# Performance work log

Hardware: AMD Instinct MI355X
Metric: run time of the kernel (lower is better)

## Reference

```python
import jax, jax.numpy as jnp
import numpy as np

B, L, E, H = 2, 2048, 1024, 16
D = E // H

def setup_inputs() -> dict:
    key = jax.random.key(0)
    ks = jax.random.split(key, 6)
    s = 1.0 / np.sqrt(E)
    return {
        "x": jax.random.normal(ks[0], (B, L, E), dtype=jnp.float32),
        "attention_mask": jnp.ones((B, L), dtype=jnp.float32),
        "Wq": jax.random.normal(ks[1], (E, E), dtype=jnp.float32) * s,
        "Wk": jax.random.normal(ks[2], (E, E), dtype=jnp.float32) * s,
        "Wv": jax.random.normal(ks[3], (E, E), dtype=jnp.float32) * s,
        "Wo": jax.random.normal(ks[4], (E, E), dtype=jnp.float32) * s,
        "bo": jnp.zeros((E,), dtype=jnp.float32),
    }

def reference(x, attention_mask, Wq, Wk, Wv, Wo, bo):
    b, l, e = x.shape
    h, d = H, D

    def proj(W):
        # (B,L,E) @ (E,E)^T -> (B,L,E) -> (B,H,L,D)
        return (x @ W.T).reshape(b, l, h, d).transpose(0, 2, 1, 3)

    q, k, v = proj(Wq), proj(Wk), proj(Wv)

    # multiplicative attention mask on q, k, v (mask shape (B,L) -> (B,1,L,1))
    m = attention_mask[:, None, :, None].astype(x.dtype)
    q, k, v = q * m, k * m, v * m

    scale = 1.0 / np.sqrt(d)
    scores = jnp.einsum('bhqd,bhkd->bhqk', q, k) * scale  # (B,H,L,L)
    causal = jnp.tril(jnp.ones((l, l), dtype=bool))
    scores = jnp.where(causal[None, None], scores, -jnp.inf)
    attn = jax.nn.softmax(scores, axis=-1)
    y = jnp.einsum('bhqk,bhkd->bhqd', attn, v)  # (B,H,L,D)
    y = y.transpose(0, 2, 1, 3).reshape(b, l, e)
    return y @ Wo.T + bo
```

## Files before the change

### kernel.cpp

```cpp
#include <hip/hip_runtime.h>
#include <cstdint>
#include <cstddef>
#include <math.h>

#define BB 2
#define LL 2048
#define EE 1024
#define HH 16
#define DD 64
#define MM (BB*LL)

typedef short short8 __attribute__((ext_vector_type(8)));
typedef float f32x4 __attribute__((ext_vector_type(4)));
typedef float f32x16 __attribute__((ext_vector_type(16)));

#define GPTR __attribute__((address_space(1)))
#define LPTR __attribute__((address_space(3)))

__device__ __forceinline__ unsigned short f32_bf16(float f) {
  union { float f; unsigned u; } c; c.f = f;
  c.u += 0x7fffu + ((c.u >> 16) & 1u);
  return (unsigned short)(c.u >> 16);
}

__device__ __forceinline__ unsigned pk_bf16(float lo, float hi) {
  unsigned r;
  asm("v_cvt_pk_bf16_f32 %0, %1, %2" : "=v"(r) : "v"(lo), "v"(hi));
  return r;
}
__device__ __forceinline__ void swap32(unsigned &a, unsigned &b) {
  asm("v_permlane32_swap_b32 %0, %1" : "+v"(a), "+v"(b));
}
__device__ __forceinline__ f32x16 zero16() {
  f32x16 v;
  #pragma unroll
  for (int e = 0; e < 16; ++e) v[e] = 0.f;
  return v;
}

__global__ void cvt_all(const float* __restrict__ x,  const float* __restrict__ wq,
                        const float* __restrict__ wk, const float* __restrict__ wv,
                        const float* __restrict__ wo,
                        unsigned short* __restrict__ xb,  unsigned short* __restrict__ wqb,
                        unsigned short* __restrict__ wkb, unsigned short* __restrict__ wvb,
                        unsigned short* __restrict__ wob)
{
  int i = (blockIdx.x * 256 + threadIdx.x) * 4;
  if (i >= MM * EE + 4 * EE * EE) return;
  const float* s; unsigned short* d; int off;
  if (i < MM * EE) { s = x; d = xb; off = i; }
  else {
    int k = i - MM * EE;
    int w = k >> 20;
    off = k & (EE * EE - 1);
    s = (w == 0) ? wq : (w == 1) ? wk : (w == 2) ? wv : wo;
    d = (w == 0) ? wqb : (w == 1) ? wkb : (w == 2) ? wvb : wob;
  }
  float4 v = *(const float4*)(s + off);
  union { unsigned short s[4]; uint2 u; } o;
  o.s[0] = f32_bf16(v.x); o.s[1] = f32_bf16(v.y);
  o.s[2] = f32_bf16(v.z); o.s[3] = f32_bf16(v.w);
  *(uint2*)(d + off) = o.u;
}

template<int MODE>
__global__ __launch_bounds__(256, 2)
void gemm128(const unsigned short* __restrict__ A,
             const unsigned short* __restrict__ W0,
             const unsigned short* __restrict__ W1,
             const unsigned short* __restrict__ W2,
             const float* __restrict__ mask,
             const float* __restrict__ bias,
             unsigned short* __restrict__ O0,
             unsigned short* __restrict__ O1,
             unsigned short* __restrict__ O2,
             float* __restrict__ OF)
{
  constexpr int K = EE;
  const int tid = threadIdx.x;
  const int lane = tid & 63;
  const int wid = tid >> 6;
  const int g = lane >> 4, li = lane & 15;
  const int m0 = blockIdx.y * 128;
  const int n0 = blockIdx.x * 128;
  const int z = blockIdx.z;

  const unsigned short* Wp = W0;
  if (MODE == 0) Wp = (z == 0) ? W0 : ((z == 1) ? W1 : W2);

  __shared__ unsigned short As[128 * 64];
  __shared__ unsigned short Bs[128 * 64];

  f32x4 acc[4][4];
  f32x4 zero = {0.f, 0.f, 0.f, 0.f};
  #pragma unroll
  for (int i = 0; i < 4; ++i)
    #pragma unroll
    for (int j = 0; j < 4; ++j) acc[i][j] = zero;

  const int wm = (wid >> 1) * 64;
  const int wn = (wid & 1) * 64;

  for (int kt = 0; kt < K; kt += 64) {
    #pragma unroll
    for (int j = 0; j < 4; ++j) {
      int c = j * 256 + tid;
      int row = c >> 3;
      int lcol = ((c & 7) * 16) ^ ((row & 7) << 4);
      __builtin_amdgcn_global_load_lds(
        (const GPTR void*)((const char*)(A + (size_t)(m0 + row) * K + kt) + lcol),
        (LPTR void*)((char*)As + c * 16), 16, 0, 0);
      __builtin_amdgcn_global_load_lds(
        (const GPTR void*)((const char*)(Wp + (size_t)(n0 + row) * K + kt) + lcol),
        (LPTR void*)((char*)Bs + c * 16), 16, 0, 0);
    }
    __syncthreads();

    #pragma unroll
    for (int kk = 0; kk < 2; ++kk) {
      short8 a[4], b[4];
      const int colb = (kk * 32 + g * 8) * 2;
      #pragma unroll
      for (int i = 0; i < 4; ++i) {
        int ar = wm + i * 16 + li;
        a[i] = *(const short8*)((const char*)As + ar * 128 + (colb ^ ((ar & 7) << 4)));
        int br = wn + i * 16 + li;
        b[i] = *(const short8*)((const char*)Bs + br * 128 + (colb ^ ((br & 7) << 4)));
      }
      #pragma unroll
      for (int i = 0; i < 4; ++i)
        #pragma unroll
        for (int j = 0; j < 4; ++j)
          acc[i][j] = __builtin_amdgcn_mfma_f32_16x16x32_bf16(a[i], b[j], acc[i][j], 0, 0, 0);
    }
    __syncthreads();
  }

  if (MODE == 0) {
    if (z == 2) {
      #pragma unroll
      for (int i = 0; i < 4; ++i) {
        int mbase = m0 + wm + i * 16 + g * 4;
        int bb2 = mbase >> 11;
        int l0  = mbase & (LL - 1);
        float mk[4];
        #pragma unroll
        for (int r = 0; r < 4; ++r) mk[r] = mask[mbase + r];
        #pragma unroll
        for (int j = 0; j < 4; ++j) {
          int n = n0 + wn + j * 16 + li;
          int h2 = n >> 6, dd2 = n & 63;
          union { unsigned short s[4]; uint2 u; } o;
          #pragma unroll
          for (int r = 0; r < 4; ++r) o.s[r] = f32_bf16(acc[i][j][r] * mk[r]);
          *(uint2*)(O2 + ((size_t)(bb2 * HH + h2) * DD + dd2) * LL + l0) = o.u;
        }
      }
    } else {
      unsigned short* Op = (z == 0) ? O0 : O1;
      const float sc = (z == 0) ? 0.125f : 1.0f;
      #pragma unroll
      for (int i = 0; i < 4; ++i) {
        #pragma unroll
        for (int r = 0; r < 4; ++r) {
          int m = m0 + wm + i * 16 + g * 4 + r;
          float mk = mask[m] * sc;
          int bb = m >> 11;
          int l  = m & (LL - 1);
          #pragma unroll
          for (int j = 0; j < 4; ++j) {
            int n = n0 + wn + j * 16 + li;
            int h = n >> 6, d = n & 63;
            size_t off = (((size_t)(bb * HH + h)) * LL + l) * DD + d;
            Op[off] = f32_bf16(acc[i][j][r] * mk);
          }
        }
      }
    }
  } else {
    #pragma unroll
    for (int i = 0; i < 4; ++i) {
      #pragma unroll
      for (int j = 0; j < 4; ++j) {
        int n = n0 + wn + j * 16 + li;
        float bv = bias[n];
        #pragma unroll
        for (int r = 0; r < 4; ++r) {
          int m = m0 + wm + i * 16 + g * 4 + r;
          OF[(size_t)m * EE + n] = acc[i][j][r] + bv;
        }
      }
    }
  }
}

__global__ __launch_bounds__(256, 2)
void attn2(const unsigned short* __restrict__ Q,
           const unsigned short* __restrict__ K,
           const unsigned short* __restrict__ VT,
           unsigned short* __restrict__ Y)
{
  const int tid = threadIdx.x, lane = tid & 63, wq = tid >> 6;
  const int l31 = lane & 31, hi = lane >> 5;
  const int qt = (int)gridDim.x - 1 - (int)blockIdx.x;
  const int q0 = qt * 128;
  const int bh = blockIdx.y;
  const int b = bh >> 4, h = bh & (HH - 1);
  const size_t kbase = (size_t)bh * LL * DD;

  __shared__ unsigned short Ks[2][64 * 64];
  __shared__ unsigned short Vs[2][64 * 64];

  const unsigned short* Kg  = K + kbase;
  const unsigned short* VTg = VT + kbase;

  const int qrow = q0 + wq * 32 + l31;
  const int qmin = q0 + wq * 32;

  short8 qf0, qf1, qf2, qf3;
  {
    const unsigned short* Qr = Q + kbase + (size_t)qrow * DD + hi * 8;
    qf0 = *(const short8*)(Qr);
    qf1 = *(const short8*)(Qr + 16);
    qf2 = *(const short8*)(Qr + 32);
    qf3 = *(const short8*)(Qr + 48);
  }

  f32x16 ot0 = zero16(), ot1 = zero16();
  float m = -INFINITY, lsum = 0.f;

  const int nt = (q0 + 128) >> 6;

  auto stage = [&](int buf, int t2) {
    const int kv0s = t2 << 6;
    #pragma unroll
    for (int u = 0; u < 2; ++u) {
      int c = u * 256 + tid;
      int row = c >> 3;
      int cb = (c & 7) * 16;
      int scol = cb ^ ((row & 7) << 4);
      __builtin_amdgcn_global_load_lds(
        (const GPTR void*)((const char*)(Kg + (size_t)(kv0s + row) * DD) + scol),
        (LPTR void*)((char*)Ks[buf] + c * 16), 16, 0, 0);
      __builtin_amdgcn_global_load_lds(
        (const GPTR void*)((const char*)(VTg + (size_t)row * LL + kv0s) + scol),
        (LPTR void*)((char*)Vs[buf] + c * 16), 16, 0, 0);
    }
  };

  stage(0, 0);
  int cur = 0;

  for (int t = 0; t < nt; ++t) {
    __syncthreads();
    if (t + 1 < nt) stage(cur ^ 1, t + 1);
    const int kv0 = t << 6;

    if (kv0 <= qmin + 31) {
      const char* Kb_ = (const char*)Ks[cur];
      const char* Vb_ = (const char*)Vs[cur];
      const int cb0 = hi * 16;
      const int r0 = l31, r1 = 32 + l31;
      const int swz = ((l31 & 7) << 4);

      f32x16 s0 = zero16(), s1 = zero16();
      #pragma unroll
      for (int kc = 0; kc < 4; ++kc) {
        int cb = kc * 32 + cb0;
        short8 k0 = *(const short8*)(Kb_ + r0 * 128 + (cb ^ swz));
        short8 k1 = *(const short8*)(Kb_ + r1 * 128 + (cb ^ swz));
        short8 qv = (kc == 0) ? qf0 : (kc == 1) ? qf1 : (kc == 2) ? qf2 : qf3;
        s0 = __builtin_amdgcn_mfma_f32_32x32x16_bf16(k0, qv, s0, 0, 0, 0);
        s1 = __builtin_amdgcn_mfma_f32_32x32x16_bf16(k1, qv, s1, 0, 0, 0);
      }

      if (kv0 + 63 > qmin) {
        #pragma unroll
        for (int rg = 0; rg < 4; ++rg)
          #pragma unroll
          for (int e = 0; e < 4; ++e) {
            int kvg = kv0 + rg * 8 + hi * 4 + e;
            if (kvg > qrow)      s0[rg * 4 + e] = -INFINITY;
            if (kvg + 32 > qrow) s1[rg * 4 + e] = -INFINITY;
          }
      }

      float mv = s0[0];
      #pragma unroll
      for (int e = 1; e < 16; ++e) mv = fmaxf(mv, s0[e]);
      #pragma unroll
      for (int e = 0; e < 16; ++e) mv = fmaxf(mv, s1[e]);
      mv = fmaxf(mv, __shfl_xor(mv, 32, 64));
      float mnew = fmaxf(m, mv);
      float al = __expf(m - mnew);
      m = mnew;
      float rs = 0.f;
      #pragma unroll
      for (int e = 0; e < 16; ++e) { s0[e] = __expf(s0[e] - mnew); rs += s0[e]; }
      #pragma unroll
      for (int e = 0; e < 16; ++e) { s1[e] = __expf(s1[e] - mnew); rs += s1[e]; }
      rs += __shfl_xor(rs, 32, 64);
      lsum = lsum * al + rs;
      #pragma unroll
      for (int e = 0; e < 16; ++e) { ot0[e] *= al; ot1[e] *= al; }

      auto mkfrag = [&](const f32x16& sv, int base) -> short8 {
        unsigned a0 = pk_bf16(sv[base + 0], sv[base + 1]);
        unsigned a1 = pk_bf16(sv[base + 2], sv[base + 3]);
        unsigned b0 = pk_bf16(sv[base + 4], sv[base + 5]);
        unsigned b1 = pk_bf16(sv[base + 6], sv[base + 7]);
        swap32(a0, b0);
        swap32(a1, b1);
        union { unsigned u[4]; short8 s; } f;
        f.u[0] = a0; f.u[1] = a1; f.u[2] = b0; f.u[3] = b1;
        return f.s;
      };
      short8 pf0 = mkfrag(s0, 0), pf1 = mkfrag(s0, 8);
      short8 pf2 = mkfrag(s1, 0), pf3 = mkfrag(s1, 8);

      #pragma unroll
      for (int kc = 0; kc < 4; ++kc) {
        int cb = kc * 32 + cb0;
        short8 v0 = *(const short8*)(Vb_ + r0 * 128 + (cb ^ swz));
        short8 v1 = *(const short8*)(Vb_ + r1 * 128 + (cb ^ swz));
        short8 pv = (kc == 0) ? pf0 : (kc == 1) ? pf1 : (kc == 2) ? pf2 : pf3;
        ot0 = __builtin_amdgcn_mfma_f32_32x32x16_bf16(v0, pv, ot0, 0, 0, 0);
        ot1 = __builtin_amdgcn_mfma_f32_32x32x16_bf16(v1, pv, ot1, 0, 0, 0);
      }
    }
    cur ^= 1;
  }

  float inv = 1.0f / lsum;
  unsigned short* Yr = Y + ((size_t)b * LL + qrow) * EE + h * DD;
  #pragma unroll
  for (int rg = 0; rg < 4; ++rg) {
    union { unsigned short s[4]; uint2 u; } o0, o1;
    #pragma unroll
    for (int e = 0; e < 4; ++e) {
      o0.s[e] = f32_bf16(ot0[rg * 4 + e] * inv);
      o1.s[e] = f32_bf16(ot1[rg * 4 + e] * inv);
    }
    *(uint2*)(Yr + rg * 8 + hi * 4) = o0.u;
    *(uint2*)(Yr + 32 + rg * 8 + hi * 4) = o1.u;
  }
}

extern "C" void kernel_launch(void* const* d_in, const int* in_sizes, int n_in,
                              void* d_out, int out_size, void* d_ws, size_t ws_size,
                              hipStream_t stream) {
  const float* x    = (const float*)d_in[0];
  const float* mask = (const float*)d_in[1];
  const float* Wq   = (const float*)d_in[2];
  const float* Wk   = (const float*)d_in[3];
  const float* Wv   = (const float*)d_in[4];
  const float* Wo   = (const float*)d_in[5];
  const float* bo   = (const float*)d_in[6];
  float* out = (float*)d_out;

  char* ws = (char*)d_ws;
  unsigned short* xb  = (unsigned short*)(ws);
  unsigned short* wqb = (unsigned short*)(ws + ((size_t)8  << 20));
  unsigned short* wkb = (unsigned short*)(ws + ((size_t)10 << 20));
  unsigned short* wvb = (unsigned short*)(ws + ((size_t)12 << 20));
  unsigned short* wob = (unsigned short*)(ws + ((size_t)14 << 20));
  unsigned short* Qb  = (unsigned short*)(ws + ((size_t)16 << 20));
  unsigned short* Kb  = (unsigned short*)(ws + ((size_t)24 << 20));
  unsigned short* VTb = (unsigned short*)(ws + ((size_t)32 << 20));
  unsigned short* Yb  = (unsigned short*)(ws + ((size_t)40 << 20));

  cvt_all<<<8192, 256, 0, stream>>>(x, Wq, Wk, Wv, Wo, xb, wqb, wkb, wvb, wob);

  gemm128<0><<<dim3(EE / 128, MM / 128, 3), 256, 0, stream>>>(
      xb, wqb, wkb, wvb, mask, nullptr, Qb, Kb, VTb, nullptr);

  attn2<<<dim3(LL / 128, BB * HH), 256, 0, stream>>>(Qb, Kb, VTb, Yb);

  gemm128<1><<<dim3(EE / 128, MM / 128, 1), 256, 0, stream>>>(
      Yb, wob, nullptr, nullptr, nullptr, bo, nullptr, nullptr, nullptr, out);
}
```

Baseline: 121.9 us.

## Shrink attention blocks to 64 queries, remap grid, add lazy rescale and setprio

The attention kernel now runs 128-thread blocks that each cover 64 query rows, launched on a flat 1024-block grid. The grid is remapped so heaviest query tiles go first and batch-heads are interleaved, which aims to improve load balance across CUs. It skips the second half of QK^T and PV MFMAs on diagonal tiles where they would be fully masked. It also adds a lazy softmax rescale (skips the correction unless the max grows by more than 8), tree reductions, and s_setprio around MFMA sections. The trade-off is more K/V LDS staging per query row, since each block reloads the full key range for only half the queries, plus some extra numeric range risk from the deferred rescale.

```diff
diff --git a/kernel.cpp b/kernel.cpp
--- a/kernel.cpp
+++ b/kernel.cpp
@@ -194,7 +194,7 @@
   }
 }
 
-__global__ __launch_bounds__(256, 2)
+__global__ __launch_bounds__(128, 2)
 void attn2(const unsigned short* __restrict__ Q,
            const unsigned short* __restrict__ K,
            const unsigned short* __restrict__ VT,
@@ -202,9 +202,13 @@
 {
   const int tid = threadIdx.x, lane = tid & 63, wq = tid >> 6;
   const int l31 = lane & 31, hi = lane >> 5;
-  const int qt = (int)gridDim.x - 1 - (int)blockIdx.x;
-  const int q0 = qt * 128;
-  const int bh = blockIdx.y;
+
+  const int id = blockIdx.x;
+  const int bh_lo = id & 7;
+  const int r_ = id >> 3;
+  const int bh = (r_ & 3) * 8 + bh_lo;
+  const int qt = 31 - (r_ >> 2);
+  const int q0 = qt * 64;
   const int b = bh >> 4, h = bh & (HH - 1);
   const size_t kbase = (size_t)bh * LL * DD;
 
@@ -229,13 +233,13 @@
   f32x16 ot0 = zero16(), ot1 = zero16();
   float m = -INFINITY, lsum = 0.f;
 
-  const int nt = (q0 + 128) >> 6;
+  const int nt = qt + 1;
 
   auto stage = [&](int buf, int t2) {
     const int kv0s = t2 << 6;
     #pragma unroll
-    for (int u = 0; u < 2; ++u) {
-      int c = u * 256 + tid;
+    for (int u = 0; u < 4; ++u) {
+      int c = u * 128 + tid;
       int row = c >> 3;
       int cb = (c & 7) * 16;
       int scol = cb ^ ((row & 7) << 4);
@@ -255,78 +259,114 @@
     __syncthreads();
     if (t + 1 < nt) stage(cur ^ 1, t + 1);
     const int kv0 = t << 6;
-
-    if (kv0 <= qmin + 31) {
-      const char* Kb_ = (const char*)Ks[cur];
-      const char* Vb_ = (const char*)Vs[cur];
-      const int cb0 = hi * 16;
-      const int r0 = l31, r1 = 32 + l31;
-      const int swz = ((l31 & 7) << 4);
-
-      f32x16 s0 = zero16(), s1 = zero16();
-      #pragma unroll
-      for (int kc = 0; kc < 4; ++kc) {
-        int cb = kc * 32 + cb0;
-        short8 k0 = *(const short8*)(Kb_ + r0 * 128 + (cb ^ swz));
+    const bool need1 = (kv0 + 32 <= qmin + 31);
+
+    const char* Kb_ = (const char*)Ks[cur];
+    const char* Vb_ = (const char*)Vs[cur];
+    const int cb0 = hi * 16;
+    const int r0 = l31, r1 = 32 + l31;
+    const int swz = ((l31 & 7) << 4);
+
+    f32x16 s0 = zero16(), s1 = zero16();
+    __builtin_amdgcn_s_setprio(1);
+    #pragma unroll
+    for (int kc = 0; kc < 4; ++kc) {
+      int cb = kc * 32 + cb0;
+      short8 k0 = *(const short8*)(Kb_ + r0 * 128 + (cb ^ swz));
+      short8 qv = (kc == 0) ? qf0 : (kc == 1) ? qf1 : (kc == 2) ? qf2 : qf3;
+      s0 = __builtin_amdgcn_mfma_f32_32x32x16_bf16(k0, qv, s0, 0, 0, 0);
+      if (need1) {
         short8 k1 = *(const short8*)(Kb_ + r1 * 128 + (cb ^ swz));
-        short8 qv = (kc == 0) ? qf0 : (kc == 1) ? qf1 : (kc == 2) ? qf2 : qf3;
-        s0 = __builtin_amdgcn_mfma_f32_32x32x16_bf16(k0, qv, s0, 0, 0, 0);
         s1 = __builtin_amdgcn_mfma_f32_32x32x16_bf16(k1, qv, s1, 0, 0, 0);
       }
-
-      if (kv0 + 63 > qmin) {
-        #pragma unroll
-        for (int rg = 0; rg < 4; ++rg)
-          #pragma unroll
-          for (int e = 0; e < 4; ++e) {
-            int kvg = kv0 + rg * 8 + hi * 4 + e;
-            if (kvg > qrow)      s0[rg * 4 + e] = -INFINITY;
-            if (kvg + 32 > qrow) s1[rg * 4 + e] = -INFINITY;
-          }
-      }
-
-      float mv = s0[0];
-      #pragma unroll
-      for (int e = 1; e < 16; ++e) mv = fmaxf(mv, s0[e]);
-      #pragma unroll
-      for (int e = 0; e < 16; ++e) mv = fmaxf(mv, s1[e]);
-      mv = fmaxf(mv, __shfl_xor(mv, 32, 64));
+    }
+    __builtin_amdgcn_s_setprio(0);
+
+    if (kv0 + 63 > qmin) {
+      #pragma unroll
+      for (int rg = 0; rg < 4; ++rg)
+        #pragma unroll
+        for (int e = 0; e < 4; ++e) {
+          int kvg = kv0 + rg * 8 + hi * 4 + e;
+          if (kvg > qrow)                s0[rg * 4 + e] = -INFINITY;
+          if (need1 && kvg + 32 > qrow)  s1[rg * 4 + e] = -INFINITY;
+        }
+    }
+
+    float red[16];
+    #pragma unroll
+    for (int e = 0; e < 16; ++e) red[e] = need1 ? fmaxf(s0[e], s1[e]) : s0[e];
+    #pragma unroll
+    for (int st = 8; st >= 1; st >>= 1)
+      #pragma unroll
+      for (int e = 0; e < 8; ++e) if (e < st) red[e] = fmaxf(red[e], red[e + st]);
+    float mv = red[0];
+    mv = fmaxf(mv, __shfl_xor(mv, 32, 64));
+
+    if (!__all(mv <= m + 8.0f)) {
       float mnew = fmaxf(m, mv);
       float al = __expf(m - mnew);
       m = mnew;
-      float rs = 0.f;
-      #pragma unroll
-      for (int e = 0; e < 16; ++e) { s0[e] = __expf(s0[e] - mnew); rs += s0[e]; }
-      #pragma unroll
-      for (int e = 0; e < 16; ++e) { s1[e] = __expf(s1[e] - mnew); rs += s1[e]; }
-      rs += __shfl_xor(rs, 32, 64);
-      lsum = lsum * al + rs;
+      lsum *= al;
       #pragma unroll
       for (int e = 0; e < 16; ++e) { ot0[e] *= al; ot1[e] *= al; }
-
-      auto mkfrag = [&](const f32x16& sv, int base) -> short8 {
-        unsigned a0 = pk_bf16(sv[base + 0], sv[base + 1]);
-        unsigned a1 = pk_bf16(sv[base + 2], sv[base + 3]);
-        unsigned b0 = pk_bf16(sv[base + 4], sv[base + 5]);
-        unsigned b1 = pk_bf16(sv[base + 6], sv[base + 7]);
-        swap32(a0, b0);
-        swap32(a1, b1);
-        union { unsigned u[4]; short8 s; } f;
-        f.u[0] = a0; f.u[1] = a1; f.u[2] = b0; f.u[3] = b1;
-        return f.s;
-      };
-      short8 pf0 = mkfrag(s0, 0), pf1 = mkfrag(s0, 8);
+    }
+
+    float rs;
+    {
+      float ra[16];
+      #pragma unroll
+      for (int e = 0; e < 16; ++e) { s0[e] = __expf(s0[e] - m); ra[e] = s0[e]; }
+      if (need1) {
+        #pragma unroll
+        for (int e = 0; e < 16; ++e) { s1[e] = __expf(s1[e] - m); ra[e] += s1[e]; }
+      }
+      #pragma unroll
+      for (int st = 8; st >= 1; st >>= 1)
+        #pragma unroll
+        for (int e = 0; e < 8; ++e) if (e < st) ra[e] += ra[e + st];
+      rs = ra[0];
+    }
+    rs += __shfl_xor(rs, 32, 64);
+    lsum += rs;
+
+    auto mkfrag = [&](const f32x16& sv, int base) -> short8 {
+      unsigned a0 = pk_bf16(sv[base + 0], sv[base + 1]);
+      unsigned a1 = pk_bf16(sv[base + 2], sv[base + 3]);
+      unsigned b0 = pk_bf16(sv[base + 4], sv[base + 5]);
+      unsigned b1 = pk_bf16(sv[base + 6], sv[base + 7]);
+      swap32(a0, b0);
+      swap32(a1, b1);
+      union { unsigned u[4]; short8 s; } f;
+      f.u[0] = a0; f.u[1] = a1; f.u[2] = b0; f.u[3] = b1;
+      return f.s;
+    };
+    short8 pf0 = mkfrag(s0, 0), pf1 = mkfrag(s0, 8);
+
+    __builtin_amdgcn_s_setprio(1);
+    #pragma unroll
+    for (int kc = 0; kc < 2; ++kc) {
+      int cb = kc * 32 + cb0;
+      short8 v0 = *(const short8*)(Vb_ + r0 * 128 + (cb ^ swz));
+      short8 v1 = *(const short8*)(Vb_ + r1 * 128 + (cb ^ swz));
+      short8 pv = (kc == 0) ? pf0 : pf1;
+      ot0 = __builtin_amdgcn_mfma_f32_32x32x16_bf16(v0, pv, ot0, 0, 0, 0);
+      ot1 = __builtin_amdgcn_mfma_f32_32x32x16_bf16(v1, pv, ot1, 0, 0, 0);
+    }
+    __builtin_amdgcn_s_setprio(0);
+    if (need1) {
       short8 pf2 = mkfrag(s1, 0), pf3 = mkfrag(s1, 8);
-
-      #pragma unroll
-      for (int kc = 0; kc < 4; ++kc) {
+      __builtin_amdgcn_s_setprio(1);
+      #pragma unroll
+      for (int kc = 2; kc < 4; ++kc) {
         int cb = kc * 32 + cb0;
         short8 v0 = *(const short8*)(Vb_ + r0 * 128 + (cb ^ swz));
         short8 v1 = *(const short8*)(Vb_ + r1 * 128 + (cb ^ swz));
-        short8 pv = (kc == 0) ? pf0 : (kc == 1) ? pf1 : (kc == 2) ? pf2 : pf3;
+        short8 pv = (kc == 2) ? pf2 : pf3;
         ot0 = __builtin_amdgcn_mfma_f32_32x32x16_bf16(v0, pv, ot0, 0, 0, 0);
         ot1 = __builtin_amdgcn_mfma_f32_32x32x16_bf16(v1, pv, ot1, 0, 0, 0);
       }
+      __builtin_amdgcn_s_setprio(0);
     }
     cur ^= 1;
   }
@@ -374,7 +414,7 @@
   gemm128<0><<<dim3(EE / 128, MM / 128, 3), 256, 0, stream>>>(
       xb, wqb, wkb, wvb, mask, nullptr, Qb, Kb, VTb, nullptr);
 
-  attn2<<<dim3(LL / 128, BB * HH), 256, 0, stream>>>(Qb, Kb, VTb, Yb);
+  attn2<<<dim3(1024), 128, 0, stream>>>(Qb, Kb, VTb, Yb);
 
   gemm128<1><<<dim3(EE / 128, MM / 128, 1), 256, 0, stream>>>(
       Yb, wob, nullptr, nullptr, nullptr, bo, nullptr, nullptr, nullptr, out);
```

After: 121.9 us. No clear change (-0.1%).
